# Performance work log

Measured on AMD Instinct MI355X. Metric: run time of the kernel, lower is better.

## Reference

```python
import jax, jax.numpy as jnp
import numpy as np

D = 1024      # d_model
H = 16        # nhead
DH = 64       # qkv_dim (per-head)
FF = 4096     # dim_feedforward
EPS = 1e-5


def layer_norm(x, g, b):
    mu = jnp.mean(x, axis=-1, keepdims=True)
    var = jnp.mean(jnp.square(x - mu), axis=-1, keepdims=True)
    return (x - mu) * jax.lax.rsqrt(var + EPS) * g + b


def setup_inputs() -> dict:
    key = jax.random.key(0)
    ks = jax.random.split(key, 17)
    s = 0.02
    inp = {
        "src": jax.random.normal(ks[0], (2, 2048, D), jnp.float32),
        "qw": jax.random.normal(ks[1], (H * DH, D), jnp.float32) * s,
        "qb": jnp.zeros((H * DH,), jnp.float32),
        "kw": jax.random.normal(ks[2], (H * DH, D), jnp.float32) * s,
        "kb": jnp.zeros((H * DH,), jnp.float32),
        "vw": jax.random.normal(ks[3], (H * DH, D), jnp.float32) * s,
        "vb": jnp.zeros((H * DH,), jnp.float32),
        "ow": jax.random.normal(ks[4], (D, H * DH), jnp.float32) * s,
        "ob": jnp.zeros((D,), jnp.float32),
        "w1": jax.random.normal(ks[5], (FF, D), jnp.float32) * s,
        "b1": jnp.zeros((FF,), jnp.float32),
        "w2": jax.random.normal(ks[6], (D, FF), jnp.float32) * s,
        "b2": jnp.zeros((D,), jnp.float32),
        "g1": jnp.ones((D,), jnp.float32),
        "beta1": jnp.zeros((D,), jnp.float32),
        "g2": jnp.ones((D,), jnp.float32),
        "beta2": jnp.zeros((D,), jnp.float32),
    }
    return inp


def _attn(x, qw, qb, kw, kb, vw, vb, ow, ob):
    B, S, _ = x.shape
    scale = 1.0 / np.sqrt(DH)
    # projections -> [B, H, S, DH]
    q = (x @ qw.T + qb).reshape(B, S, H, DH).transpose(0, 2, 1, 3)
    k = (x @ kw.T + kb).reshape(B, S, H, DH).transpose(0, 2, 1, 3)
    v = (x @ vw.T + vb).reshape(B, S, H, DH).transpose(0, 2, 1, 3)
    scores = jnp.einsum('bhsd,bhtd->bhst', q, k) * scale
    attn = jax.nn.softmax(scores, axis=-1)
    out = jnp.einsum('bhst,bhtd->bhsd', attn, v)  # [B,H,S,DH]
    out = out.transpose(0, 2, 1, 3).reshape(B, S, H * DH)
    return out @ ow.T + ob


def reference(src, qw, qb, kw, kb, vw, vb, ow, ob, w1, b1, w2, b2, g1, beta1, g2, beta2):
    x = src
    # post-LN (norm_first=False), dropout=0 (eval)
    x = layer_norm(x + _attn(x, qw, qb, kw, kb, vw, vb, ow, ob), g1, beta1)
    ff = jax.nn.relu(x @ w1.T + b1) @ w2.T + b2
    x = layer_norm(x + ff, g2, beta2)
    return x
```

## Files before the change

kernel.cpp:

```cpp
#include <hip/hip_runtime.h>

typedef unsigned short bf16_t;
typedef unsigned short u16x8 __attribute__((ext_vector_type(8)));
typedef unsigned short u16x4 __attribute__((ext_vector_type(4)));
typedef float f32x4 __attribute__((ext_vector_type(4)));

#define D_MODEL 1024
#define NHEAD 16
#define DHEAD 64
#define FF_DIM 4096
#define SEQ 2048
#define BATCH 2
#define LOG2E 1.44269504088896340736f
#define EXP2F(x) __builtin_amdgcn_exp2f(x)

#define GLOAD_LDS16(gp, lp)                                          \
  __builtin_amdgcn_global_load_lds(                                  \
      (const __attribute__((address_space(1))) void*)(gp),           \
      (__attribute__((address_space(3))) void*)(lp), 16, 0, 0)

static __device__ __forceinline__ float bf2f(bf16_t b) {
  union { unsigned u; float f; } x;
  x.u = ((unsigned)b) << 16;
  return x.f;
}
static __device__ __forceinline__ bf16_t f2bf(float f) {
  union { float f; unsigned u; } x;
  x.f = f;
  unsigned r = (x.u + 0x7fffu + ((x.u >> 16) & 1u)) >> 16;
  return (bf16_t)r;
}
static __device__ __forceinline__ int cvtpk(float lo, float hi) {
  int r;
  asm("v_cvt_pk_bf16_f32 %0, %1, %2" : "=v"(r) : "v"(lo), "v"(hi));
  return r;
}
static __device__ __forceinline__ f32x4 mfma16(u16x8 a, u16x8 b, f32x4 c) {
  return __builtin_amdgcn_mfma_f32_16x16x32_bf16(a, b, c, 0, 0, 0);
}
static __device__ __forceinline__ u16x8 load8_f32(const float* q) {
  const float4 v0 = *(const float4*)(q);
  const float4 v1 = *(const float4*)(q + 4);
  u16x8 r;
  r[0] = f2bf(v0.x); r[1] = f2bf(v0.y); r[2] = f2bf(v0.z); r[3] = f2bf(v0.w);
  r[4] = f2bf(v1.x); r[5] = f2bf(v1.y); r[6] = f2bf(v1.z); r[7] = f2bf(v1.w);
  return r;
}

__global__ __launch_bounds__(256) void cvt_f32_bf16(
    const float* __restrict__ in, bf16_t* __restrict__ out, long n) {
  const long i = ((long)blockIdx.x * 256 + threadIdx.x) * 8;
  if (i < n) *(u16x8*)(out + i) = load8_f32(in + i);
}

template <int BM, int SMODE>
__global__ __launch_bounds__(256) void gemm_lds(
    const bf16_t* __restrict__ A, const bf16_t* __restrict__ W,
    const float* __restrict__ bq_, const float* __restrict__ bk_,
    const float* __restrict__ bv_, bf16_t* __restrict__ C0,
    bf16_t* __restrict__ C1, bf16_t* __restrict__ C2,
    float* __restrict__ CP0, float* __restrict__ CP1,
    int M, int N, int Kseg, long lda, long ldw, int relu, float qscale) {
  constexpr int WM = BM / 2;
  constexpr int MI = WM / 16;
  __shared__ bf16_t As[BM * 32];
  __shared__ bf16_t Bs[128 * 32];
  const int tid = threadIdx.x;
  const int lane = tid & 63;
  const int w = tid >> 6;
  const int wr = w >> 1, wc = w & 1;
  const int g = lane >> 4, c = lane & 15;
  const long bm = (long)blockIdx.y * BM;
  const long bn = (long)blockIdx.x * 128;
  const long koff = (long)blockIdx.z * Kseg;

  f32x4 acc[MI][4];
#pragma unroll
  for (int i = 0; i < MI; ++i)
#pragma unroll
    for (int j = 0; j < 4; ++j) acc[i][j] = (f32x4){0.f, 0.f, 0.f, 0.f};

  for (int k0 = 0; k0 < Kseg; k0 += 32) {
    __syncthreads();
#pragma unroll
    for (int ld = 0; ld < BM / 64; ++ld) {
      const int ch = ld * 256 + tid;
      GLOAD_LDS16(A + (bm + (ch >> 2)) * lda + koff + k0 + (ch & 3) * 8,
                  As + (ld * 256 + w * 64) * 8);
    }
#pragma unroll
    for (int ld = 0; ld < 2; ++ld) {
      const int ch = ld * 256 + tid;
      GLOAD_LDS16(W + (bn + (ch >> 2)) * ldw + koff + k0 + (ch & 3) * 8,
                  Bs + (ld * 256 + w * 64) * 8);
    }
    __syncthreads();
    u16x8 af[MI], bfv[4];
#pragma unroll
    for (int i = 0; i < MI; ++i)
      af[i] = *(const u16x8*)(As + (wr * WM + i * 16 + c) * 32 + g * 8);
#pragma unroll
    for (int j = 0; j < 4; ++j)
      bfv[j] = *(const u16x8*)(Bs + (wc * 64 + j * 16 + c) * 32 + g * 8);
    __builtin_amdgcn_s_setprio(1);
#pragma unroll
    for (int i = 0; i < MI; ++i)
#pragma unroll
      for (int j = 0; j < 4; ++j) acc[i][j] = mfma16(af[i], bfv[j], acc[i][j]);
    __builtin_amdgcn_s_setprio(0);
  }

  float* __restrict__ cp = blockIdx.z ? CP1 : CP0;
#pragma unroll
  for (int i = 0; i < MI; ++i) {
#pragma unroll
    for (int j = 0; j < 4; ++j) {
      const int nn = (int)bn + wc * 64 + j * 16 + c;
#pragma unroll
      for (int r = 0; r < 4; ++r) {
        const int mm = (int)bm + wr * WM + i * 16 + g * 4 + r;
        if (SMODE == 0) {
          float v = acc[i][j][r] + bq_[nn];
          if (relu) v = fmaxf(v, 0.f);
          C0[(long)mm * N + nn] = f2bf(v);
        } else if (SMODE == 4) {
          cp[(long)mm * N + nn] = acc[i][j][r];
        } else {
          const int seg = nn >> 10;
          const int col = nn & 1023;
          const int h = col >> 6, dh = col & 63;
          const int b = mm >> 11, s = mm & 2047;
          if (seg == 0) {
            const float v = (acc[i][j][r] + bq_[col]) * qscale;
            C0[((((long)b * NHEAD + h) * SEQ + s) << 6) + dh] = f2bf(v);
          } else if (seg == 1) {
            const float v = acc[i][j][r] + bk_[col];
            C1[((((long)b * NHEAD + h) * SEQ + s) << 6) + dh] = f2bf(v);
          } else {
            const float v = acc[i][j][r] + bv_[col];
            C2[(((long)b * NHEAD + h) * DHEAD + dh) * SEQ + s] = f2bf(v);
          }
        }
      }
    }
  }
}

static __device__ __forceinline__ void stage_tile(
    const bf16_t* __restrict__ gbase, long rstride, bf16_t* lds,
    int tid, int w) {
#pragma unroll
  for (int i = 0; i < 2; ++i) {
    const int row = i * 32 + (tid >> 3);
    const int c4 = (tid & 7) ^ (row & 7);
    GLOAD_LDS16(gbase + (long)row * rstride + c4 * 8,
                lds + (i * 256 + w * 64) * 8);
  }
}

__global__ __launch_bounds__(256, 4) void attn_fwd(
    const bf16_t* __restrict__ Q, const bf16_t* __restrict__ K,
    const bf16_t* __restrict__ Vt, bf16_t* __restrict__ O) {
  __shared__ bf16_t Ks0[64 * 64];
  __shared__ bf16_t Ks1[64 * 64];
  __shared__ bf16_t Vs0[64 * 64];
  __shared__ bf16_t Vs1[64 * 64];
  const int tid = threadIdx.x;
  const int lane = tid & 63;
  const int w = tid >> 6;
  const int g = lane >> 4, c = lane & 15;
  const int lb = blockIdx.x;
  const int xcd = lb & 7, sl = lb >> 3;
  const int bh = xcd * 4 + (sl >> 5);
  const int q0 = (sl & 31) * 64 + w * 16;
  const bf16_t* Qb = Q + (long)bh * SEQ * DHEAD;
  const bf16_t* Kb = K + (long)bh * SEQ * DHEAD;
  const bf16_t* Vb = Vt + (long)bh * DHEAD * SEQ;

  const u16x8 bq0 = *(const u16x8*)(Qb + (q0 + c) * DHEAD + g * 8);
  const u16x8 bq1 = *(const u16x8*)(Qb + (q0 + c) * DHEAD + 32 + g * 8);

  float m = -1e30f, lp = 0.f;
  f32x4 oacc[4];
#pragma unroll
  for (int d = 0; d < 4; ++d) oacc[d] = (f32x4){0.f, 0.f, 0.f, 0.f};

  const int srcA = c + 16 * (2 * (g & 1));
  const int srcH = srcA + 16;
  const bool glo2 = (g < 2);
  const int cx = c & 7;

  for (int t0 = 0; t0 < SEQ; t0 += 128) {
    __syncthreads();
    stage_tile(Kb + (long)t0 * DHEAD, DHEAD, Ks0, tid, w);
    stage_tile(Kb + (long)(t0 + 64) * DHEAD, DHEAD, Ks1, tid, w);
    stage_tile(Vb + t0, SEQ, Vs0, tid, w);
    stage_tile(Vb + t0 + 64, SEQ, Vs1, tid, w);
    __syncthreads();

#pragma unroll
    for (int sub = 0; sub < 2; ++sub) {
      const bf16_t* Ks = sub ? Ks1 : Ks0;
      const bf16_t* Vs = sub ? Vs1 : Vs0;

      u16x8 kf[8];
#pragma unroll
      for (int tt = 0; tt < 4; ++tt) {
        const int rowb = (tt * 16 + c) * 64;
        kf[tt * 2 + 0] = *(const u16x8*)(Ks + rowb + ((g ^ cx)) * 8);
        kf[tt * 2 + 1] = *(const u16x8*)(Ks + rowb + (((4 + g) ^ cx)) * 8);
      }
      f32x4 s[4];
      __builtin_amdgcn_s_setprio(1);
#pragma unroll
      for (int tt = 0; tt < 4; ++tt) {
        s[tt] = mfma16(kf[tt * 2 + 0], bq0, (f32x4){0.f, 0.f, 0.f, 0.f});
        s[tt] = mfma16(kf[tt * 2 + 1], bq1, s[tt]);
      }
      __builtin_amdgcn_s_setprio(0);

      float pm = s[0][0];
#pragma unroll
      for (int tt = 0; tt < 4; ++tt)
#pragma unroll
        for (int r = 0; r < 4; ++r) pm = fmaxf(pm, s[tt][r]);
      pm = fmaxf(pm, __shfl_xor(pm, 16));
      pm = fmaxf(pm, __shfl_xor(pm, 32));
      if (!__all(pm <= m + 8.f)) {
        const float mn = fmaxf(m, pm);
        const float f = EXP2F(m - mn);
        m = mn;
        lp *= f;
        float fb[4];
#pragma unroll
        for (int r = 0; r < 4; ++r) fb[r] = __shfl(f, 4 * g + r);
#pragma unroll
        for (int d = 0; d < 4; ++d)
#pragma unroll
          for (int r = 0; r < 4; ++r) oacc[d][r] *= fb[r];
      }
      float p[16];
#pragma unroll
      for (int tt = 0; tt < 4; ++tt)
#pragma unroll
        for (int r = 0; r < 4; ++r) p[tt * 4 + r] = EXP2F(s[tt][r] - m);
      float ts = 0.f;
#pragma unroll
      for (int i = 0; i < 16; ++i) ts += p[i];
      lp += ts;

      int wd[8];
#pragma unroll
      for (int tt = 0; tt < 4; ++tt) {
        wd[tt * 2 + 0] = cvtpk(p[tt * 4 + 0], p[tt * 4 + 1]);
        wd[tt * 2 + 1] = cvtpk(p[tt * 4 + 2], p[tt * 4 + 3]);
      }
      union { int u[4]; u16x8 v; } pu0, pu1;
      pu0.u[0] = glo2 ? __shfl(wd[0], srcA) : __shfl(wd[2], srcA);
      pu0.u[1] = glo2 ? __shfl(wd[1], srcA) : __shfl(wd[3], srcA);
      pu0.u[2] = glo2 ? __shfl(wd[0], srcH) : __shfl(wd[2], srcH);
      pu0.u[3] = glo2 ? __shfl(wd[1], srcH) : __shfl(wd[3], srcH);
      pu1.u[0] = glo2 ? __shfl(wd[4], srcA) : __shfl(wd[6], srcA);
      pu1.u[1] = glo2 ? __shfl(wd[5], srcA) : __shfl(wd[7], srcA);
      pu1.u[2] = glo2 ? __shfl(wd[4], srcH) : __shfl(wd[6], srcH);
      pu1.u[3] = glo2 ? __shfl(wd[5], srcH) : __shfl(wd[7], srcH);

      __builtin_amdgcn_s_setprio(1);
#pragma unroll
      for (int d = 0; d < 4; ++d) {
        const int rowb = (d * 16 + c) * 64;
        const u16x8 v0 = *(const u16x8*)(Vs + rowb + ((g ^ cx)) * 8);
        const u16x8 v1 = *(const u16x8*)(Vs + rowb + (((4 + g) ^ cx)) * 8);
        oacc[d] = mfma16(pu0.v, v0, oacc[d]);
        oacc[d] = mfma16(pu1.v, v1, oacc[d]);
      }
      __builtin_amdgcn_s_setprio(0);
    }
  }

  float lt = lp;
  lt += __shfl_xor(lt, 16);
  lt += __shfl_xor(lt, 32);
  const int b = bh >> 4, h = bh & 15;
#pragma unroll
  for (int r = 0; r < 4; ++r) {
    const float inv = 1.f / __shfl(lt, 4 * g + r);
    const long base = ((long)b * SEQ + q0 + g * 4 + r) * D_MODEL + h * DHEAD;
#pragma unroll
    for (int d = 0; d < 4; ++d) O[base + d * 16 + c] = f2bf(oacc[d][r] * inv);
  }
}

template <int XF32, int OUTF32, int YPART>
__global__ __launch_bounds__(256) void add_ln(
    const void* __restrict__ X, const bf16_t* __restrict__ Ybf,
    const float* __restrict__ P0, const float* __restrict__ P1,
    const float* __restrict__ ybias,
    const float* __restrict__ gamma, const float* __restrict__ beta,
    void* __restrict__ Out) {
  __shared__ float red[2][4];
  const int tid = threadIdx.x;
  const int lane = tid & 63, w = tid >> 6;
  const long base = (long)blockIdx.x * D_MODEL;

  float xv[4];
  if (XF32) {
    const float4 t = *(const float4*)((const float*)X + base + tid * 4);
    xv[0] = t.x; xv[1] = t.y; xv[2] = t.z; xv[3] = t.w;
  } else {
    const u16x4 t = *(const u16x4*)((const bf16_t*)X + base + tid * 4);
#pragma unroll
    for (int i = 0; i < 4; ++i) xv[i] = bf2f(t[i]);
  }
  float yv[4];
  if (YPART) {
    const float4 p0 = *(const float4*)(P0 + base + tid * 4);
    const float4 p1 = *(const float4*)(P1 + base + tid * 4);
    const float4 bb = *(const float4*)(ybias + tid * 4);
    yv[0] = p0.x + p1.x + bb.x;
    yv[1] = p0.y + p1.y + bb.y;
    yv[2] = p0.z + p1.z + bb.z;
    yv[3] = p0.w + p1.w + bb.w;
  } else {
    const u16x4 t = *(const u16x4*)(Ybf + base + tid * 4);
#pragma unroll
    for (int i = 0; i < 4; ++i) yv[i] = bf2f(t[i]);
  }
  float v[4], s = 0.f, s2 = 0.f;
#pragma unroll
  for (int i = 0; i < 4; ++i) {
    const float t = xv[i] + yv[i];
    v[i] = t;
    s += t;
    s2 += t * t;
  }
#pragma unroll
  for (int off = 32; off; off >>= 1) {
    s += __shfl_xor(s, off);
    s2 += __shfl_xor(s2, off);
  }
  if (lane == 0) { red[0][w] = s; red[1][w] = s2; }
  __syncthreads();
  s = red[0][0] + red[0][1] + red[0][2] + red[0][3];
  s2 = red[1][0] + red[1][1] + red[1][2] + red[1][3];
  const float mu = s * (1.f / D_MODEL);
  const float var = s2 * (1.f / D_MODEL) - mu * mu;
  const float inv = rsqrtf(var + 1e-5f);
  const float4 gv = *(const float4*)(gamma + tid * 4);
  const float4 bv = *(const float4*)(beta + tid * 4);
  const float o0 = (v[0] - mu) * inv * gv.x + bv.x;
  const float o1 = (v[1] - mu) * inv * gv.y + bv.y;
  const float o2 = (v[2] - mu) * inv * gv.z + bv.z;
  const float o3 = (v[3] - mu) * inv * gv.w + bv.w;
  if (OUTF32) {
    float4 ov; ov.x = o0; ov.y = o1; ov.z = o2; ov.w = o3;
    *(float4*)((float*)Out + base + tid * 4) = ov;
  } else {
    u16x4 ov;
    ov[0] = f2bf(o0); ov[1] = f2bf(o1); ov[2] = f2bf(o2); ov[3] = f2bf(o3);
    *(u16x4*)((bf16_t*)Out + base + tid * 4) = ov;
  }
}

extern "C" void kernel_launch(void* const* d_in, const int* in_sizes, int n_in,
                              void* d_out, int out_size, void* d_ws, size_t ws_size,
                              hipStream_t stream) {
  const float* src = (const float*)d_in[0];
  const float* qw = (const float*)d_in[1];
  const float* qb = (const float*)d_in[2];
  const float* kw = (const float*)d_in[3];
  const float* kb = (const float*)d_in[4];
  const float* vw = (const float*)d_in[5];
  const float* vb = (const float*)d_in[6];
  const float* ow = (const float*)d_in[7];
  const float* ob = (const float*)d_in[8];
  const float* w1 = (const float*)d_in[9];
  const float* b1 = (const float*)d_in[10];
  const float* w2 = (const float*)d_in[11];
  const float* b2 = (const float*)d_in[12];
  const float* gam1 = (const float*)d_in[13];
  const float* bet1 = (const float*)d_in[14];
  const float* gam2 = (const float*)d_in[15];
  const float* bet2 = (const float*)d_in[16];

  char* ws = (char*)d_ws;
  const long MB = 1024 * 1024;
  bf16_t* Qw   = (bf16_t*)(ws + 0 * MB);
  bf16_t* Kw   = (bf16_t*)(ws + 8 * MB);
  bf16_t* Vt   = (bf16_t*)(ws + 16 * MB);
  bf16_t* A1   = (bf16_t*)(ws + 24 * MB);
  float*  Po0  = (float*)(ws + 0 * MB);
  float*  Po1  = (float*)(ws + 80 * MB);
  bf16_t* X1   = (bf16_t*)(ws + 40 * MB);
  bf16_t* srcB = (bf16_t*)(ws + 48 * MB);
  bf16_t* Wqkv = (bf16_t*)(ws + 56 * MB);
  bf16_t* OWb  = (bf16_t*)(ws + 62 * MB);
  bf16_t* W1b  = (bf16_t*)(ws + 64 * MB);
  bf16_t* W2b  = (bf16_t*)(ws + 72 * MB);
  bf16_t* F1   = (bf16_t*)(ws + 0 * MB);
  float*  P0   = (float*)(ws + 48 * MB);
  float*  P1   = (float*)(ws + 80 * MB);

  const int M = BATCH * SEQ;
  dim3 blk(256);
  const float qscale = 0.125f * LOG2E;
  const long n1M = 1024 * 1024;

  cvt_f32_bf16<<<dim3(2048), blk, 0, stream>>>(src, srcB, (long)M * D_MODEL);
  cvt_f32_bf16<<<dim3(512), blk, 0, stream>>>(qw, Wqkv, n1M);
  cvt_f32_bf16<<<dim3(512), blk, 0, stream>>>(kw, Wqkv + n1M, n1M);
  cvt_f32_bf16<<<dim3(512), blk, 0, stream>>>(vw, Wqkv + 2 * n1M, n1M);
  cvt_f32_bf16<<<dim3(512), blk, 0, stream>>>(ow, OWb, n1M);
  cvt_f32_bf16<<<dim3(2048), blk, 0, stream>>>(w1, W1b, 4 * n1M);
  cvt_f32_bf16<<<dim3(2048), blk, 0, stream>>>(w2, W2b, 4 * n1M);

  gemm_lds<128, 3><<<dim3(24, 32, 1), blk, 0, stream>>>(
      srcB, Wqkv, qb, kb, vb, Qw, Kw, Vt, (float*)0, (float*)0,
      M, 3072, 1024, 1024, 1024, 0, qscale);
  attn_fwd<<<dim3(1024), blk, 0, stream>>>(Qw, Kw, Vt, A1);
  gemm_lds<128, 4><<<dim3(8, 32, 2), blk, 0, stream>>>(
      A1, OWb, ob, ob, ob, (bf16_t*)0, (bf16_t*)0, (bf16_t*)0, Po0, Po1,
      M, 1024, 512, 1024, 1024, 0, 1.f);
  add_ln<1, 0, 1><<<dim3(M), blk, 0, stream>>>(
      src, (const bf16_t*)0, Po0, Po1, ob, gam1, bet1, X1);
  gemm_lds<128, 0><<<dim3(32, 32, 1), blk, 0, stream>>>(
      X1, W1b, b1, b1, b1, F1, F1, F1, (float*)0, (float*)0,
      M, 4096, 1024, 1024, 1024, 1, 1.f);
  gemm_lds<128, 4><<<dim3(8, 32, 2), blk, 0, stream>>>(
      F1, W2b, b2, b2, b2, (bf16_t*)0, (bf16_t*)0, (bf16_t*)0, P0, P1,
      M, 1024, 2048, 4096, 4096, 0, 1.f);
  add_ln<0, 1, 1><<<dim3(M), blk, 0, stream>>>(
      X1, (const bf16_t*)0, P0, P1, b2, gam2, bet2, d_out);
}
```

Baseline: 296.7 us.

## Process two query sub-tiles per wave in attention to reuse K/V fragments

Each wave in the attention kernel now handles 32 query rows (two 16-row groups) instead of 16, so every K and V fragment read from LDS feeds twice as many MFMAs. The grid is halved and launch bounds drop to 2 blocks per SM. The K tile gets a different XOR swizzle plus a row permutation, so the score MFMA outputs line up with the P operand layout of the PV MFMA, which removes the cross-lane shuffles that rebuilt P before. The costs are higher register pressure and fewer resident waves to hide latency.

```diff
diff --git a/kernel.cpp b/kernel.cpp
--- a/kernel.cpp
+++ b/kernel.cpp
@@ -146,19 +146,21 @@
   }
 }
 
+template <int KEY>
 static __device__ __forceinline__ void stage_tile(
     const bf16_t* __restrict__ gbase, long rstride, bf16_t* lds,
     int tid, int w) {
 #pragma unroll
   for (int i = 0; i < 2; ++i) {
     const int row = i * 32 + (tid >> 3);
-    const int c4 = (tid & 7) ^ (row & 7);
+    const int key = KEY ? ((row & 3) | ((row & 8) >> 1)) : (row & 7);
+    const int c4 = (tid & 7) ^ key;
     GLOAD_LDS16(gbase + (long)row * rstride + c4 * 8,
                 lds + (i * 256 + w * 64) * 8);
   }
 }
 
-__global__ __launch_bounds__(256, 4) void attn_fwd(
+__global__ __launch_bounds__(256, 2) void attn_fwd(
     const bf16_t* __restrict__ Q, const bf16_t* __restrict__ K,
     const bf16_t* __restrict__ Vt, bf16_t* __restrict__ O) {
   __shared__ bf16_t Ks0[64 * 64];
@@ -171,31 +173,35 @@
   const int g = lane >> 4, c = lane & 15;
   const int lb = blockIdx.x;
   const int xcd = lb & 7, sl = lb >> 3;
-  const int bh = xcd * 4 + (sl >> 5);
-  const int q0 = (sl & 31) * 64 + w * 16;
+  const int bh = xcd * 4 + (sl >> 4);
+  const int q0 = (sl & 15) * 128 + w * 32;
   const bf16_t* Qb = Q + (long)bh * SEQ * DHEAD;
   const bf16_t* Kb = K + (long)bh * SEQ * DHEAD;
   const bf16_t* Vb = Vt + (long)bh * DHEAD * SEQ;
 
-  const u16x8 bq0 = *(const u16x8*)(Qb + (q0 + c) * DHEAD + g * 8);
-  const u16x8 bq1 = *(const u16x8*)(Qb + (q0 + c) * DHEAD + 32 + g * 8);
-
-  float m = -1e30f, lp = 0.f;
-  f32x4 oacc[4];
-#pragma unroll
-  for (int d = 0; d < 4; ++d) oacc[d] = (f32x4){0.f, 0.f, 0.f, 0.f};
-
-  const int srcA = c + 16 * (2 * (g & 1));
-  const int srcH = srcA + 16;
-  const bool glo2 = (g < 2);
-  const int cx = c & 7;
+  u16x8 bq[2][2];
+#pragma unroll
+  for (int qh = 0; qh < 2; ++qh) {
+    bq[qh][0] = *(const u16x8*)(Qb + (q0 + qh * 16 + c) * DHEAD + g * 8);
+    bq[qh][1] = *(const u16x8*)(Qb + (q0 + qh * 16 + c) * DHEAD + 32 + g * 8);
+  }
+
+  float m0 = -1e30f, m1 = -1e30f, lp0 = 0.f, lp1 = 0.f;
+  f32x4 oacc[4][2];
+#pragma unroll
+  for (int d = 0; d < 4; ++d)
+#pragma unroll
+    for (int qh = 0; qh < 2; ++qh) oacc[d][qh] = (f32x4){0.f, 0.f, 0.f, 0.f};
+
+  const int ck = c & 7;
+  const int pr = ((c >> 2) << 3) | (c & 3);
 
   for (int t0 = 0; t0 < SEQ; t0 += 128) {
     __syncthreads();
-    stage_tile(Kb + (long)t0 * DHEAD, DHEAD, Ks0, tid, w);
-    stage_tile(Kb + (long)(t0 + 64) * DHEAD, DHEAD, Ks1, tid, w);
-    stage_tile(Vb + t0, SEQ, Vs0, tid, w);
-    stage_tile(Vb + t0 + 64, SEQ, Vs1, tid, w);
+    stage_tile<1>(Kb + (long)t0 * DHEAD, DHEAD, Ks0, tid, w);
+    stage_tile<1>(Kb + (long)(t0 + 64) * DHEAD, DHEAD, Ks1, tid, w);
+    stage_tile<0>(Vb + t0, SEQ, Vs0, tid, w);
+    stage_tile<0>(Vb + t0 + 64, SEQ, Vs1, tid, w);
     __syncthreads();
 
 #pragma unroll
@@ -203,91 +209,117 @@
       const bf16_t* Ks = sub ? Ks1 : Ks0;
       const bf16_t* Vs = sub ? Vs1 : Vs0;
 
-      u16x8 kf[8];
-#pragma unroll
-      for (int tt = 0; tt < 4; ++tt) {
-        const int rowb = (tt * 16 + c) * 64;
-        kf[tt * 2 + 0] = *(const u16x8*)(Ks + rowb + ((g ^ cx)) * 8);
-        kf[tt * 2 + 1] = *(const u16x8*)(Ks + rowb + (((4 + g) ^ cx)) * 8);
+      f32x4 s[2][2][2];
+#pragma unroll
+      for (int tt = 0; tt < 2; ++tt) {
+        const int rowA = (tt * 32 + pr) * 64;
+        const int rowC = (tt * 32 + pr + 4) * 64;
+        const u16x8 kA = *(const u16x8*)(Ks + rowA + (g ^ ck) * 8);
+        const u16x8 kB = *(const u16x8*)(Ks + rowA + ((4 + g) ^ ck) * 8);
+        const u16x8 kC = *(const u16x8*)(Ks + rowC + (g ^ ck) * 8);
+        const u16x8 kD = *(const u16x8*)(Ks + rowC + ((4 + g) ^ ck) * 8);
+        __builtin_amdgcn_s_setprio(1);
+#pragma unroll
+        for (int qh = 0; qh < 2; ++qh) {
+          s[tt][0][qh] = mfma16(kA, bq[qh][0], (f32x4){0.f, 0.f, 0.f, 0.f});
+          s[tt][0][qh] = mfma16(kB, bq[qh][1], s[tt][0][qh]);
+          s[tt][1][qh] = mfma16(kC, bq[qh][0], (f32x4){0.f, 0.f, 0.f, 0.f});
+          s[tt][1][qh] = mfma16(kD, bq[qh][1], s[tt][1][qh]);
+        }
+        __builtin_amdgcn_s_setprio(0);
       }
-      f32x4 s[4];
-      __builtin_amdgcn_s_setprio(1);
-#pragma unroll
-      for (int tt = 0; tt < 4; ++tt) {
-        s[tt] = mfma16(kf[tt * 2 + 0], bq0, (f32x4){0.f, 0.f, 0.f, 0.f});
-        s[tt] = mfma16(kf[tt * 2 + 1], bq1, s[tt]);
+
+      float pmv[2];
+#pragma unroll
+      for (int qh = 0; qh < 2; ++qh) {
+        float pm = s[0][0][qh][0];
+#pragma unroll
+        for (int tt = 0; tt < 2; ++tt)
+#pragma unroll
+          for (int pi = 0; pi < 2; ++pi)
+#pragma unroll
+            for (int r = 0; r < 4; ++r) pm = fmaxf(pm, s[tt][pi][qh][r]);
+        pm = fmaxf(pm, __shfl_xor(pm, 16));
+        pm = fmaxf(pm, __shfl_xor(pm, 32));
+        pmv[qh] = pm;
       }
-      __builtin_amdgcn_s_setprio(0);
-
-      float pm = s[0][0];
-#pragma unroll
-      for (int tt = 0; tt < 4; ++tt)
-#pragma unroll
-        for (int r = 0; r < 4; ++r) pm = fmaxf(pm, s[tt][r]);
-      pm = fmaxf(pm, __shfl_xor(pm, 16));
-      pm = fmaxf(pm, __shfl_xor(pm, 32));
-      if (!__all(pm <= m + 8.f)) {
-        const float mn = fmaxf(m, pm);
-        const float f = EXP2F(m - mn);
-        m = mn;
-        lp *= f;
-        float fb[4];
-#pragma unroll
-        for (int r = 0; r < 4; ++r) fb[r] = __shfl(f, 4 * g + r);
+      if (!__all(pmv[0] <= m0 + 8.f && pmv[1] <= m1 + 8.f)) {
+        const float mn0 = fmaxf(m0, pmv[0]);
+        const float mn1 = fmaxf(m1, pmv[1]);
+        const float f0 = EXP2F(m0 - mn0);
+        const float f1 = EXP2F(m1 - mn1);
+        m0 = mn0; m1 = mn1;
+        lp0 *= f0; lp1 *= f1;
+        float fb0[4], fb1[4];
+#pragma unroll
+        for (int r = 0; r < 4; ++r) {
+          fb0[r] = __shfl(f0, 4 * g + r);
+          fb1[r] = __shfl(f1, 4 * g + r);
+        }
 #pragma unroll
         for (int d = 0; d < 4; ++d)
 #pragma unroll
-          for (int r = 0; r < 4; ++r) oacc[d][r] *= fb[r];
+          for (int r = 0; r < 4; ++r) {
+            oacc[d][0][r] *= fb0[r];
+            oacc[d][1][r] *= fb1[r];
+          }
       }
-      float p[16];
-#pragma unroll
-      for (int tt = 0; tt < 4; ++tt)
-#pragma unroll
-        for (int r = 0; r < 4; ++r) p[tt * 4 + r] = EXP2F(s[tt][r] - m);
-      float ts = 0.f;
-#pragma unroll
-      for (int i = 0; i < 16; ++i) ts += p[i];
-      lp += ts;
-
-      int wd[8];
-#pragma unroll
-      for (int tt = 0; tt < 4; ++tt) {
-        wd[tt * 2 + 0] = cvtpk(p[tt * 4 + 0], p[tt * 4 + 1]);
-        wd[tt * 2 + 1] = cvtpk(p[tt * 4 + 2], p[tt * 4 + 3]);
-      }
-      union { int u[4]; u16x8 v; } pu0, pu1;
-      pu0.u[0] = glo2 ? __shfl(wd[0], srcA) : __shfl(wd[2], srcA);
-      pu0.u[1] = glo2 ? __shfl(wd[1], srcA) : __shfl(wd[3], srcA);
-      pu0.u[2] = glo2 ? __shfl(wd[0], srcH) : __shfl(wd[2], srcH);
-      pu0.u[3] = glo2 ? __shfl(wd[1], srcH) : __shfl(wd[3], srcH);
-      pu1.u[0] = glo2 ? __shfl(wd[4], srcA) : __shfl(wd[6], srcA);
-      pu1.u[1] = glo2 ? __shfl(wd[5], srcA) : __shfl(wd[7], srcA);
-      pu1.u[2] = glo2 ? __shfl(wd[4], srcH) : __shfl(wd[6], srcH);
-      pu1.u[3] = glo2 ? __shfl(wd[5], srcH) : __shfl(wd[7], srcH);
-
-      __builtin_amdgcn_s_setprio(1);
+      float ts0 = 0.f, ts1 = 0.f;
+#pragma unroll
+      for (int tt = 0; tt < 2; ++tt)
+#pragma unroll
+        for (int pi = 0; pi < 2; ++pi)
+#pragma unroll
+          for (int r = 0; r < 4; ++r) {
+            s[tt][pi][0][r] = EXP2F(s[tt][pi][0][r] - m0);
+            s[tt][pi][1][r] = EXP2F(s[tt][pi][1][r] - m1);
+            ts0 += s[tt][pi][0][r];
+            ts1 += s[tt][pi][1][r];
+          }
+      lp0 += ts0;
+      lp1 += ts1;
+
+      union { int u[4]; u16x8 v; } pu[2][2];
+#pragma unroll
+      for (int qh = 0; qh < 2; ++qh)
+#pragma unroll
+        for (int tt = 0; tt < 2; ++tt) {
+          pu[qh][tt].u[0] = cvtpk(s[tt][0][qh][0], s[tt][0][qh][1]);
+          pu[qh][tt].u[1] = cvtpk(s[tt][0][qh][2], s[tt][0][qh][3]);
+          pu[qh][tt].u[2] = cvtpk(s[tt][1][qh][0], s[tt][1][qh][1]);
+          pu[qh][tt].u[3] = cvtpk(s[tt][1][qh][2], s[tt][1][qh][3]);
+        }
+
 #pragma unroll
       for (int d = 0; d < 4; ++d) {
         const int rowb = (d * 16 + c) * 64;
-        const u16x8 v0 = *(const u16x8*)(Vs + rowb + ((g ^ cx)) * 8);
-        const u16x8 v1 = *(const u16x8*)(Vs + rowb + (((4 + g) ^ cx)) * 8);
-        oacc[d] = mfma16(pu0.v, v0, oacc[d]);
-        oacc[d] = mfma16(pu1.v, v1, oacc[d]);
+        const u16x8 v0 = *(const u16x8*)(Vs + rowb + ((g ^ ck)) * 8);
+        const u16x8 v1 = *(const u16x8*)(Vs + rowb + (((4 + g) ^ ck)) * 8);
+        __builtin_amdgcn_s_setprio(1);
+        oacc[d][0] = mfma16(pu[0][0].v, v0, oacc[d][0]);
+        oacc[d][0] = mfma16(pu[0][1].v, v1, oacc[d][0]);
+        oacc[d][1] = mfma16(pu[1][0].v, v0, oacc[d][1]);
+        oacc[d][1] = mfma16(pu[1][1].v, v1, oacc[d][1]);
+        __builtin_amdgcn_s_setprio(0);
       }
-      __builtin_amdgcn_s_setprio(0);
     }
   }
 
-  float lt = lp;
-  lt += __shfl_xor(lt, 16);
-  lt += __shfl_xor(lt, 32);
   const int b = bh >> 4, h = bh & 15;
 #pragma unroll
-  for (int r = 0; r < 4; ++r) {
-    const float inv = 1.f / __shfl(lt, 4 * g + r);
-    const long base = ((long)b * SEQ + q0 + g * 4 + r) * D_MODEL + h * DHEAD;
-#pragma unroll
-    for (int d = 0; d < 4; ++d) O[base + d * 16 + c] = f2bf(oacc[d][r] * inv);
+  for (int qh = 0; qh < 2; ++qh) {
+    float lt = qh ? lp1 : lp0;
+    lt += __shfl_xor(lt, 16);
+    lt += __shfl_xor(lt, 32);
+#pragma unroll
+    for (int r = 0; r < 4; ++r) {
+      const float inv = 1.f / __shfl(lt, 4 * g + r);
+      const long base =
+          ((long)b * SEQ + q0 + qh * 16 + g * 4 + r) * D_MODEL + h * DHEAD;
+#pragma unroll
+      for (int d = 0; d < 4; ++d)
+        O[base + d * 16 + c] = f2bf(oacc[d][qh][r] * inv);
+    }
   }
 }
 
@@ -417,7 +449,7 @@
   gemm_lds<128, 3><<<dim3(24, 32, 1), blk, 0, stream>>>(
       srcB, Wqkv, qb, kb, vb, Qw, Kw, Vt, (float*)0, (float*)0,
       M, 3072, 1024, 1024, 1024, 0, qscale);
-  attn_fwd<<<dim3(1024), blk, 0, stream>>>(Qw, Kw, Vt, A1);
+  attn_fwd<<<dim3(512), blk, 0, stream>>>(Qw, Kw, Vt, A1);
   gemm_lds<128, 4><<<dim3(8, 32, 2), blk, 0, stream>>>(
       A1, OWb, ob, ob, ob, (bf16_t*)0, (bf16_t*)0, (bf16_t*)0, Po0, Po1,
       M, 1024, 512, 1024, 1024, 0, 1.f);
```

New measurement: 280.2 us. 1.06x faster.
